# Kernel tuning notes

Measured on AMD Instinct MI355X. Metric: run time of the kernel, lower is better.

The kernel has to match this reference:

```python
import jax, jax.numpy as jnp
import numpy as np

P_CHAN, P_FEAT = 7, 2
S_CHAN, S_FEAT = 2, 4
STATE_SIZE = 8
E, H = 32, 4
ACTIONS = 7
B = 131072


def _lin(x, w, b):
    return x @ w.T + b


def _ln(x, g, b):
    mu = jnp.mean(x, axis=-1, keepdims=True)
    var = jnp.var(x, axis=-1, keepdims=True)
    return (x - mu) * jax.lax.rsqrt(var + 1e-5) * g + b


def _encoder(x, qkv_w, qkv_b, o_w, o_b, g1, b1, f1w, f1b, f2w, f2b, g2, b2):
    # torch.nn.TransformerEncoderLayer, post-norm, relu, dropout=0
    Bn, S, Em = x.shape
    D = Em // H
    qkv = _lin(x, qkv_w, qkv_b)                      # [B,S,3E]
    q, k, v = jnp.split(qkv, 3, axis=-1)
    q = q.reshape(Bn, S, H, D).transpose(0, 2, 1, 3)  # [B,H,S,D]
    k = k.reshape(Bn, S, H, D).transpose(0, 2, 1, 3)
    v = v.reshape(Bn, S, H, D).transpose(0, 2, 1, 3)
    scores = jnp.einsum('bhsd,bhtd->bhst', q, k) * (1.0 / np.sqrt(D))
    att = jax.nn.softmax(scores, axis=-1)
    o = jnp.einsum('bhst,bhtd->bhsd', att, v).transpose(0, 2, 1, 3).reshape(Bn, S, Em)
    x = _ln(x + _lin(o, o_w, o_b), g1, b1)
    ff = _lin(jax.nn.relu(_lin(x, f1w, f1b)), f2w, f2b)
    return _ln(x + ff, g2, b2)


_BRANCH_NAMES = ['in_w', 'in_b', 'qkv_w', 'qkv_b', 'o_w', 'o_b', 'ln1_g', 'ln1_b',
                 'ff1_w', 'ff1_b', 'ff2_w', 'ff2_b', 'ln2_g', 'ln2_b', 'out_w', 'out_b']


def _branch_params(ks, feat, chan):
    def W(shape):
        s = 1.0 / np.sqrt(shape[-1])
        return jax.random.uniform(next(ks), shape, jnp.float32, -s, s)
    return [W((E, feat)), W((E,)), W((3 * E, E)), W((3 * E,)), W((E, E)), W((E,)),
            jnp.ones(E, jnp.float32), jnp.zeros(E, jnp.float32),
            W((E, E)), W((E,)), W((E, E)), W((E,)),
            jnp.ones(E, jnp.float32), jnp.zeros(E, jnp.float32),
            W((128, chan * E)), W((128,))]


def setup_inputs() -> dict:
    key = jax.random.key(0)
    ks = iter(jax.random.split(key, 64))
    def W(shape):
        s = 1.0 / np.sqrt(shape[-1])
        return jax.random.uniform(next(ks), shape, jnp.float32, -s, s)
    d = {'state': jax.random.normal(next(ks), (B, P_CHAN * P_FEAT + S_CHAN * S_FEAT + STATE_SIZE), jnp.float32)}
    d.update({f'pw_{n}': v for n, v in zip(_BRANCH_NAMES, _branch_params(ks, P_FEAT, P_CHAN))})
    d.update({f'sw_{n}': v for n, v in zip(_BRANCH_NAMES, _branch_params(ks, S_FEAT, S_CHAN))})
    d.update(dict(e_w=W((128, STATE_SIZE)), e_b=W((128,)),
                  d1_w=W((128, 384)), d1_b=W((128,)),
                  d2_w=W((128, 128)), d2_b=W((128,)),
                  pi_w=W((ACTIONS, 128)), pi_b=W((ACTIONS,)),
                  v_w=W((1, 128)), v_b=W((1,))))
    return d


def reference(state, pw_in_w, pw_in_b, pw_qkv_w, pw_qkv_b, pw_o_w, pw_o_b, pw_ln1_g, pw_ln1_b,
              pw_ff1_w, pw_ff1_b, pw_ff2_w, pw_ff2_b, pw_ln2_g, pw_ln2_b, pw_out_w, pw_out_b,
              sw_in_w, sw_in_b, sw_qkv_w, sw_qkv_b, sw_o_w, sw_o_b, sw_ln1_g, sw_ln1_b,
              sw_ff1_w, sw_ff1_b, sw_ff2_w, sw_ff2_b, sw_ln2_g, sw_ln2_b, sw_out_w, sw_out_b,
              e_w, e_b, d1_w, d1_b, d2_w, d2_b, pi_w, pi_b, v_w, v_b):
    Bn = state.shape[0]
    power, sword, ps = jnp.split(state, [P_CHAN * P_FEAT, P_CHAN * P_FEAT + S_CHAN * S_FEAT], axis=1)

    p = _lin(power.reshape(Bn * P_CHAN, P_FEAT), pw_in_w, pw_in_b).reshape(Bn, P_CHAN, E)
    p = _encoder(p, pw_qkv_w, pw_qkv_b, pw_o_w, pw_o_b, pw_ln1_g, pw_ln1_b,
                 pw_ff1_w, pw_ff1_b, pw_ff2_w, pw_ff2_b, pw_ln2_g, pw_ln2_b)
    p_emb = jax.nn.relu(_lin(p.reshape(Bn, -1), pw_out_w, pw_out_b))

    s = _lin(sword.reshape(Bn * S_CHAN, S_FEAT), sw_in_w, sw_in_b).reshape(Bn, S_CHAN, E)
    s = _encoder(s, sw_qkv_w, sw_qkv_b, sw_o_w, sw_o_b, sw_ln1_g, sw_ln1_b,
                 sw_ff1_w, sw_ff1_b, sw_ff2_w, sw_ff2_b, sw_ln2_g, sw_ln2_b)
    s_emb = jax.nn.relu(_lin(s.reshape(Bn, -1), sw_out_w, sw_out_b))

    st_emb = jax.nn.relu(_lin(ps, e_w, e_b))
    x = jnp.concatenate([p_emb, s_emb, st_emb], axis=1)  # [B,384]
    x = jax.nn.relu(_lin(x, d1_w, d1_b))
    x = jax.nn.relu(_lin(x, d2_w, d2_b))
    return jax.nn.softmax(_lin(x, pi_w, pi_b), axis=-1), _lin(x, v_w, v_b)
```

## Files before the change

### kernel.cpp

```cpp
#include <hip/hip_runtime.h>


typedef __bf16 bhalf;
typedef __bf16 bhalf4 __attribute__((ext_vector_type(4)));
typedef __bf16 bhalf8 __attribute__((ext_vector_type(8)));
typedef float f32x4 __attribute__((ext_vector_type(4)));
typedef float f32x2 __attribute__((ext_vector_type(2)));

#define DEV static __device__ __forceinline__

DEV f32x4 mfma16(bhalf8 a, bhalf8 b, f32x4 c) {
  return __builtin_amdgcn_mfma_f32_16x16x32_bf16(a, b, c, 0, 0, 0);
}

struct Ptrs {
  const float* state;
  const float *p_g1, *p_b1, *p_f1b, *p_f2b, *p_g2, *p_b2, *p_out_b;
  const float *s_g1, *s_b1, *s_f1b, *s_f2b, *s_g2, *s_b2, *s_out_b;
  const float *d1_b, *d2_b, *pi_w, *pi_b, *v_w, *v_b;
  const bhalf *A_qp, *A_xp, *w_o, *w_f1, *w_f2, *w_out;
  const bhalf *A_qs, *A_xs, *w_o2, *w_f12, *w_f22, *w_out2;
  const bhalf *A_e, *w_d1, *w_d2;
  float* out;
};

struct PrepArgs {
  const float* src[10];
  int len[10];
  int dstOff[10];
  bhalf* dst;
};

__global__ void prep_convert(PrepArgs a) {
  int idx = blockIdx.x * blockDim.x + threadIdx.x;
  int off = 0;
#pragma unroll
  for (int i = 0; i < 10; ++i) {
    int n = a.len[i];
    if (idx >= off && idx < off + n) a.dst[a.dstOff[i] + idx - off] = (bhalf)a.src[i][idx - off];
    off += n;
  }
}

struct EffArgs {
  const float *p_qkv_w, *p_in_w, *p_in_b, *p_qkv_b, *p_o_b;
  const float *s_qkv_w, *s_in_w, *s_in_b, *s_qkv_b, *s_o_b;
  const float *e_w, *e_b;
  bhalf* dst;
};

__global__ void prep_eff(EffArgs a) {
  int tid = threadIdx.x;
  if (tid < 96) {
    const float* wq = a.p_qkv_w + tid * 32;
    float w0 = 0.f, w1 = 0.f, be = 0.f;
    for (int e = 0; e < 32; ++e) {
      w0 += wq[e] * a.p_in_w[e * 2];
      w1 += wq[e] * a.p_in_w[e * 2 + 1];
      be += wq[e] * a.p_in_b[e];
    }
    be += a.p_qkv_b[tid];
    bhalf* d = a.dst + tid * 32;
    for (int k = 0; k < 32; ++k) d[k] = (bhalf)0.f;
    d[0] = (bhalf)w0; d[1] = (bhalf)w1; d[2] = (bhalf)be;
  } else if (tid < 192) {
    int o = tid - 96;
    const float* wq = a.s_qkv_w + o * 32;
    float wf[4] = {0.f, 0.f, 0.f, 0.f}, be = 0.f;
    for (int e = 0; e < 32; ++e) {
      for (int f = 0; f < 4; ++f) wf[f] += wq[e] * a.s_in_w[e * 4 + f];
      be += wq[e] * a.s_in_b[e];
    }
    be += a.s_qkv_b[o];
    bhalf* d = a.dst + 35840 + o * 32;
    for (int k = 0; k < 32; ++k) d[k] = (bhalf)0.f;
    for (int f = 0; f < 4; ++f) d[f] = (bhalf)wf[f];
    d[4] = (bhalf)be;
  } else if (tid < 224) {
    int e = tid - 192;
    bhalf* d = a.dst + 3072 + e * 32;
    for (int k = 0; k < 32; ++k) d[k] = (bhalf)0.f;
    d[0] = (bhalf)a.p_in_w[e * 2];
    d[1] = (bhalf)a.p_in_w[e * 2 + 1];
    d[2] = (bhalf)(a.p_in_b[e] + a.p_o_b[e]);
  } else if (tid < 256) {
    int e = tid - 224;
    bhalf* d = a.dst + 38912 + e * 32;
    for (int k = 0; k < 32; ++k) d[k] = (bhalf)0.f;
    for (int f = 0; f < 4; ++f) d[f] = (bhalf)a.s_in_w[e * 4 + f];
    d[4] = (bhalf)(a.s_in_b[e] + a.s_o_b[e]);
  } else if (tid < 384) {
    int o = tid - 256;
    bhalf* d = a.dst + 51200 + o * 32;
    for (int k = 0; k < 32; ++k) d[k] = (bhalf)0.f;
    for (int k = 0; k < 8; ++k) d[k] = (bhalf)a.e_w[o * 8 + k];
    d[8] = (bhalf)a.e_b[o];
  }
}

template <int T>
DEV bhalf8 attn_head(const bhalf* qkv, int rowbase, int a, int s, int h) {
  const bhalf* base = &qkv[(rowbase + s) * 104 + h * 8];
  const int rstep = 32 * 104;
  bhalf8 kf[T];
#pragma unroll
  for (int b = 0; b < T; ++b) kf[b] = *(const bhalf8*)(base + b * rstep + 32);
  bhalf8 qv = *(const bhalf8*)(base + a * rstep);
  float q[8];
#pragma unroll
  for (int i = 0; i < 8; ++i) q[i] = (float)qv[i];
  float sc[T];
  float mx = -1e30f;
#pragma unroll
  for (int b = 0; b < T; ++b) {
    float d = 0.f;
#pragma unroll
    for (int i = 0; i < 8; ++i) d += q[i] * (float)kf[b][i];
    d *= 0.35355339059327378f;
    sc[b] = d;
    mx = fmaxf(mx, d);
  }
  bhalf8 vf[T];
#pragma unroll
  for (int b = 0; b < T; ++b) vf[b] = *(const bhalf8*)(base + b * rstep + 64);
  float sum = 0.f;
#pragma unroll
  for (int b = 0; b < T; ++b) { sc[b] = __expf(sc[b] - mx); sum += sc[b]; }
  float inv = 1.f / sum;
  float o[8] = {0.f, 0.f, 0.f, 0.f, 0.f, 0.f, 0.f, 0.f};
#pragma unroll
  for (int b = 0; b < T; ++b) {
    float w = sc[b] * inv;
#pragma unroll
    for (int i = 0; i < 8; ++i) o[i] += w * (float)vf[b][i];
  }
  bhalf8 ov;
#pragma unroll
  for (int i = 0; i < 8; ++i) ov[i] = (bhalf)o[i];
  return ov;
}

DEV void ln_pass(int tid, const bhalf* src, bhalf* dst,
                 const float* gp, const float* bp, const float* gs, const float* bs) {
  for (int i = tid; i < 576; i += 512) {
    int row = i >> 1, half = i & 1;
    const bhalf* p = &src[row * 32 + half * 16];
    bhalf8 a0 = *(const bhalf8*)p;
    bhalf8 a1 = *(const bhalf8*)(p + 8);
    float v[16];
#pragma unroll
    for (int k = 0; k < 8; ++k) { v[k] = (float)a0[k]; v[8 + k] = (float)a1[k]; }
    float sum = 0.f, ss = 0.f;
#pragma unroll
    for (int k = 0; k < 16; ++k) { sum += v[k]; ss += v[k] * v[k]; }
    sum += __shfl_xor(sum, 1);
    ss += __shfl_xor(ss, 1);
    float mu = sum * 0.03125f;
    float rs = rsqrtf(ss * 0.03125f - mu * mu + 1e-5f);
    const float* g = (row < 224 ? gp : gs) + half * 16;
    const float* b = (row < 224 ? bp : bs) + half * 16;
    bhalf8 o0, o1;
#pragma unroll
    for (int k = 0; k < 8; ++k) {
      o0[k] = (bhalf)((v[k] - mu) * rs * g[k] + b[k]);
      o1[k] = (bhalf)((v[8 + k] - mu) * rs * g[8 + k] + b[8 + k]);
    }
    bhalf* q = &dst[row * 32 + half * 16];
    *(bhalf8*)q = o0;
    *(bhalf8*)(q + 8) = o1;
  }
}

__launch_bounds__(512, 4)
__global__ void aac_main(Ptrs P) {
  __shared__ __align__(16) bhalf s_x[288 * 32];
  __shared__ __align__(16) bhalf s_q[288 * 104];

  bhalf* ff1 = s_q;
  bhalf* xcat = s_q;
  bhalf* h1 = s_q + 13056;
  float* h2 = (float*)(s_q + 17408);

  const int tid = threadIdx.x;
  const int wave = tid >> 6, lane = tid & 63;
  const int l15 = lane & 15, lq = lane >> 4;
  const int s0 = blockIdx.x * 32;

  for (int f = wave; f < 144; f += 8) {
    int tile, n;
    bool isQ = f < 108;
    if (isQ) { tile = f / 6; n = f - tile * 6; }
    else { int g = f - 108; tile = g >> 1; n = g & 1; }
    bhalf8 bf;
#pragma unroll
    for (int k = 0; k < 8; ++k) bf[k] = (bhalf)0.f;
    if (lq == 0) {
      if (tile < 14) {
        int t = tile >> 1, s = (tile & 1) * 16 + l15;
        f32x2 v = *(const f32x2*)&P.state[(size_t)(s0 + s) * 30 + 2 * t];
        bf[0] = (bhalf)v[0]; bf[1] = (bhalf)v[1]; bf[2] = (bhalf)1.0f;
      } else {
        int g2 = tile - 14, ts = g2 >> 1, s = (g2 & 1) * 16 + l15;
        const float* st = &P.state[(size_t)(s0 + s) * 30 + 14 + 4 * ts];
        f32x2 v0 = *(const f32x2*)st;
        f32x2 v1 = *(const f32x2*)(st + 2);
        bf[0] = (bhalf)v0[0]; bf[1] = (bhalf)v0[1];
        bf[2] = (bhalf)v1[0]; bf[3] = (bhalf)v1[1];
        bf[4] = (bhalf)1.0f;
      }
    }
    const bhalf* aptr;
    if (isQ) aptr = (tile < 14 ? P.A_qp : P.A_qs) + (n * 16 + l15) * 32 + lq * 8;
    else     aptr = (tile < 14 ? P.A_xp : P.A_xs) + (n * 16 + l15) * 32 + lq * 8;
    f32x4 c = {0.f, 0.f, 0.f, 0.f};
    c = mfma16(*(const bhalf8*)aptr, bf, c);
    bhalf4 o;
#pragma unroll
    for (int j = 0; j < 4; ++j) o[j] = (bhalf)c[j];
    int row = tile * 16 + l15;
    if (isQ) *(bhalf4*)&s_q[row * 104 + n * 16 + lq * 4] = o;
    else     *(bhalf4*)&s_x[row * 32 + n * 16 + lq * 4] = o;
  }
  __syncthreads();

  for (int tile = wave; tile < 18; tile += 8) {
    bhalf8 ov;
    const bhalf* wo;
    if (tile < 14) {
      ov = attn_head<7>(s_q, 0, tile >> 1, (tile & 1) * 16 + l15, lq);
      wo = P.w_o;
    } else {
      int g = tile - 14;
      ov = attn_head<2>(s_q, 224, g >> 1, (g & 1) * 16 + l15, lq);
      wo = P.w_o2;
    }
    int row = tile * 16 + l15;
    bhalf4 x0 = *(const bhalf4*)&s_x[row * 32 + lq * 4];
    bhalf4 x1 = *(const bhalf4*)&s_x[row * 32 + 16 + lq * 4];
    f32x4 c0, c1;
#pragma unroll
    for (int j = 0; j < 4; ++j) { c0[j] = (float)x0[j]; c1[j] = (float)x1[j]; }
    c0 = mfma16(*(const bhalf8*)&wo[l15 * 32 + lq * 8], ov, c0);
    c1 = mfma16(*(const bhalf8*)&wo[(16 + l15) * 32 + lq * 8], ov, c1);
    bhalf4 p0, p1;
#pragma unroll
    for (int j = 0; j < 4; ++j) { p0[j] = (bhalf)c0[j]; p1[j] = (bhalf)c1[j]; }
    *(bhalf4*)&s_x[row * 32 + lq * 4] = p0;
    *(bhalf4*)&s_x[row * 32 + 16 + lq * 4] = p1;
  }
  __syncthreads();

  ln_pass(tid, s_x, s_x, P.p_g1, P.p_b1, P.s_g1, P.s_b1);
  __syncthreads();

  for (int tile = wave; tile < 18; tile += 8) {
    const bhalf* wf = tile < 14 ? P.w_f1 : P.w_f12;
    const float* fb = tile < 14 ? P.p_f1b : P.s_f1b;
    int row = tile * 16 + l15;
    bhalf8 bfr = *(const bhalf8*)&s_x[row * 32 + lq * 8];
    f32x4 c0 = {0.f, 0.f, 0.f, 0.f}, c1 = {0.f, 0.f, 0.f, 0.f};
    c0 = mfma16(*(const bhalf8*)&wf[l15 * 32 + lq * 8], bfr, c0);
    c1 = mfma16(*(const bhalf8*)&wf[(16 + l15) * 32 + lq * 8], bfr, c1);
    f32x4 b0 = *(const f32x4*)&fb[lq * 4], b1 = *(const f32x4*)&fb[16 + lq * 4];
    bhalf4 p0, p1;
#pragma unroll
    for (int j = 0; j < 4; ++j) {
      p0[j] = (bhalf)fmaxf(c0[j] + b0[j], 0.f);
      p1[j] = (bhalf)fmaxf(c1[j] + b1[j], 0.f);
    }
    *(bhalf4*)&ff1[row * 32 + lq * 4] = p0;
    *(bhalf4*)&ff1[row * 32 + 16 + lq * 4] = p1;
  }
  __syncthreads();

  for (int tile = wave; tile < 18; tile += 8) {
    const bhalf* wf = tile < 14 ? P.w_f2 : P.w_f22;
    const float* fb = tile < 14 ? P.p_f2b : P.s_f2b;
    int row = tile * 16 + l15;
    bhalf8 bfr = *(const bhalf8*)&ff1[row * 32 + lq * 8];
    bhalf4 r0 = *(const bhalf4*)&s_x[row * 32 + lq * 4];
    bhalf4 r1 = *(const bhalf4*)&s_x[row * 32 + 16 + lq * 4];
    f32x4 b0 = *(const f32x4*)&fb[lq * 4], b1 = *(const f32x4*)&fb[16 + lq * 4];
    f32x4 c0, c1;
#pragma unroll
    for (int j = 0; j < 4; ++j) {
      c0[j] = b0[j] + (float)r0[j];
      c1[j] = b1[j] + (float)r1[j];
    }
    c0 = mfma16(*(const bhalf8*)&wf[l15 * 32 + lq * 8], bfr, c0);
    c1 = mfma16(*(const bhalf8*)&wf[(16 + l15) * 32 + lq * 8], bfr, c1);
    bhalf4 p0, p1;
#pragma unroll
    for (int j = 0; j < 4; ++j) { p0[j] = (bhalf)c0[j]; p1[j] = (bhalf)c1[j]; }
    *(bhalf4*)&ff1[row * 32 + lq * 4] = p0;
    *(bhalf4*)&ff1[row * 32 + 16 + lq * 4] = p1;
  }
  __syncthreads();

  ln_pass(tid, ff1, s_x, P.p_g2, P.p_b2, P.s_g2, P.s_b2);
  __syncthreads();

  for (int f = wave; f < 48; f += 8) {
    if (f < 16) {
      int n = f >> 1, m = f & 1;
      f32x4 c = {0.f, 0.f, 0.f, 0.f};
#pragma unroll
      for (int t = 0; t < 7; ++t) {
        bhalf8 a = *(const bhalf8*)&P.w_out[(n * 16 + l15) * 224 + t * 32 + lq * 8];
        bhalf8 b = *(const bhalf8*)&s_x[(t * 32 + m * 16 + l15) * 32 + lq * 8];
        c = mfma16(a, b, c);
      }
      int oc = n * 16 + lq * 4;
      f32x4 bias = *(const f32x4*)&P.p_out_b[oc];
      bhalf4 o;
#pragma unroll
      for (int j = 0; j < 4; ++j) o[j] = (bhalf)fmaxf(c[j] + bias[j], 0.f);
      *(bhalf4*)&xcat[(m * 16 + l15) * 408 + oc] = o;
    } else if (f < 32) {
      int g = f - 16, n = g >> 1, m = g & 1;
      f32x4 c = {0.f, 0.f, 0.f, 0.f};
#pragma unroll
      for (int t = 0; t < 2; ++t) {
        bhalf8 a = *(const bhalf8*)&P.w_out2[(n * 16 + l15) * 64 + t * 32 + lq * 8];
        bhalf8 b = *(const bhalf8*)&s_x[(224 + t * 32 + m * 16 + l15) * 32 + lq * 8];
        c = mfma16(a, b, c);
      }
      int oc = n * 16 + lq * 4;
      f32x4 bias = *(const f32x4*)&P.s_out_b[oc];
      bhalf4 o;
#pragma unroll
      for (int j = 0; j < 4; ++j) o[j] = (bhalf)fmaxf(c[j] + bias[j], 0.f);
      *(bhalf4*)&xcat[(m * 16 + l15) * 408 + 128 + oc] = o;
    } else {
      int g = f - 32, n = g >> 1, m = g & 1;
      int s = m * 16 + l15;
      bhalf8 bf;
#pragma unroll
      for (int k = 0; k < 8; ++k) bf[k] = (bhalf)0.f;
      if (lq == 0) {
        const float* st = &P.state[(size_t)(s0 + s) * 30 + 22];
#pragma unroll
        for (int k = 0; k < 4; ++k) {
          f32x2 v = *(const f32x2*)(st + 2 * k);
          bf[2 * k] = (bhalf)v[0];
          bf[2 * k + 1] = (bhalf)v[1];
        }
      } else if (lq == 1) {
        bf[0] = (bhalf)1.0f;
      }
      bhalf8 a = *(const bhalf8*)&P.A_e[(n * 16 + l15) * 32 + lq * 8];
      f32x4 c = {0.f, 0.f, 0.f, 0.f};
      c = mfma16(a, bf, c);
      bhalf4 o;
#pragma unroll
      for (int j = 0; j < 4; ++j) o[j] = (bhalf)fmaxf(c[j], 0.f);
      *(bhalf4*)&xcat[s * 408 + 256 + n * 16 + lq * 4] = o;
    }
  }
  __syncthreads();

  for (int f = wave; f < 16; f += 8) {
    int m = f >> 3, n = f & 7;
    f32x4 c = {0.f, 0.f, 0.f, 0.f};
#pragma unroll
    for (int ks = 0; ks < 12; ++ks) {
      bhalf8 a = *(const bhalf8*)&P.w_d1[(n * 16 + l15) * 384 + ks * 32 + lq * 8];
      bhalf8 b = *(const bhalf8*)&xcat[(m * 16 + l15) * 408 + ks * 32 + lq * 8];
      c = mfma16(a, b, c);
    }
    int oc = n * 16 + lq * 4;
    f32x4 bias = *(const f32x4*)&P.d1_b[oc];
    bhalf4 o;
#pragma unroll
    for (int j = 0; j < 4; ++j) o[j] = (bhalf)fmaxf(c[j] + bias[j], 0.f);
    *(bhalf4*)&h1[(m * 16 + l15) * 136 + oc] = o;
  }
  __syncthreads();

  for (int f = wave; f < 16; f += 8) {
    int m = f >> 3, n = f & 7;
    f32x4 c = {0.f, 0.f, 0.f, 0.f};
#pragma unroll
    for (int ks = 0; ks < 4; ++ks) {
      bhalf8 a = *(const bhalf8*)&P.w_d2[(n * 16 + l15) * 128 + ks * 32 + lq * 8];
      bhalf8 b = *(const bhalf8*)&h1[(m * 16 + l15) * 136 + ks * 32 + lq * 8];
      c = mfma16(a, b, c);
    }
    int oc = n * 16 + lq * 4;
    f32x4 bias = *(const f32x4*)&P.d2_b[oc];
    f32x4 o;
#pragma unroll
    for (int j = 0; j < 4; ++j) o[j] = fmaxf(c[j] + bias[j], 0.f);
    *(f32x4*)&h2[(m * 16 + l15) * 140 + oc] = o;
  }
  __syncthreads();

  if (tid < 256) {
    int s = tid >> 3, o = tid & 7;
    const float* wrow = (o < 7) ? &P.pi_w[o * 128] : P.v_w;
    const float* hrow = &h2[s * 140];
    float acc = (o < 7) ? P.pi_b[o] : P.v_b[0];
#pragma unroll
    for (int k = 0; k < 32; ++k) {
      f32x4 wv = *(const f32x4*)&wrow[k * 4];
      f32x4 hv = *(const f32x4*)&hrow[k * 4];
#pragma unroll
      for (int j = 0; j < 4; ++j) acc += wv[j] * hv[j];
    }
    float xm = (o < 7) ? acc : -1e30f;
#pragma unroll
    for (int m = 1; m < 8; m <<= 1) xm = fmaxf(xm, __shfl_xor(xm, m));
    float e = (o < 7) ? __expf(acc - xm) : 0.f;
    float se = e;
#pragma unroll
    for (int m = 1; m < 8; m <<= 1) se += __shfl_xor(se, m);
    if (o < 7) P.out[(size_t)(s0 + s) * 7 + o] = e / se;
    else       P.out[917504 + s0 + s] = acc;
  }
}

extern "C" void kernel_launch(void* const* d_in, const int* in_sizes, int n_in,
                              void* d_out, int out_size, void* d_ws, size_t ws_size,
                              hipStream_t stream) {
  (void)in_sizes; (void)n_in; (void)out_size; (void)ws_size;
  const float* const* in = (const float* const*)d_in;
  bhalf* wbf = (bhalf*)d_ws;

  PrepArgs pa;
  const int srcIdx[10] = {5, 9, 11, 15, 21, 25, 27, 31, 35, 37};
  const int lens[10] = {1024, 1024, 1024, 28672, 1024, 1024, 1024, 8192, 49152, 16384};
  const int dsts[10] = {4096, 5120, 6144, 7168, 39936, 40960, 41984, 43008, 55296, 104448};
  for (int i = 0; i < 10; ++i) { pa.src[i] = in[srcIdx[i]]; pa.len[i] = lens[i]; pa.dstOff[i] = dsts[i]; }
  pa.dst = wbf;
  hipLaunchKernelGGL(prep_convert, dim3(424), dim3(256), 0, stream, pa);

  EffArgs ea;
  ea.p_qkv_w = in[3]; ea.p_in_w = in[1]; ea.p_in_b = in[2]; ea.p_qkv_b = in[4]; ea.p_o_b = in[6];
  ea.s_qkv_w = in[19]; ea.s_in_w = in[17]; ea.s_in_b = in[18]; ea.s_qkv_b = in[20]; ea.s_o_b = in[22];
  ea.e_w = in[33]; ea.e_b = in[34];
  ea.dst = wbf;
  hipLaunchKernelGGL(prep_eff, dim3(1), dim3(384), 0, stream, ea);

  Ptrs P;
  P.state = in[0];
  P.p_g1 = in[7];  P.p_b1 = in[8];  P.p_f1b = in[10]; P.p_f2b = in[12];
  P.p_g2 = in[13]; P.p_b2 = in[14]; P.p_out_b = in[16];
  P.s_g1 = in[23]; P.s_b1 = in[24]; P.s_f1b = in[26]; P.s_f2b = in[28];
  P.s_g2 = in[29]; P.s_b2 = in[30]; P.s_out_b = in[32];
  P.d1_b = in[36]; P.d2_b = in[38];
  P.pi_w = in[39]; P.pi_b = in[40]; P.v_w = in[41]; P.v_b = in[42];
  P.A_qp = wbf;          P.A_xp = wbf + 3072;   P.w_o = wbf + 4096;
  P.w_f1 = wbf + 5120;   P.w_f2 = wbf + 6144;   P.w_out = wbf + 7168;
  P.A_qs = wbf + 35840;  P.A_xs = wbf + 38912;  P.w_o2 = wbf + 39936;
  P.w_f12 = wbf + 40960; P.w_f22 = wbf + 41984; P.w_out2 = wbf + 43008;
  P.A_e = wbf + 51200;   P.w_d1 = wbf + 55296;  P.w_d2 = wbf + 104448;
  P.out = (float*)d_out;

  hipLaunchKernelGGL(aac_main, dim3(4096), dim3(512), 0, stream, P);
}
```

Measured before the change: 334.6 us.

## Fuse per-tile encoder stages into one wave-local pass with swizzled LDS

Merges attention output projection, LayerNorm 1, FF1, FF2 and LayerNorm 2 into a single per-tile routine that each wave runs on its own 16-row tile. LayerNorm is computed from the MFMA accumulators with cross-lane shuffles instead of a separate block-wide pass. This removes four block-wide __syncthreads and the intermediate LDS round trips. It also XOR-swizzles the s_x layout to reduce bank conflicts and statically unrolls the later output-projection and dense loops per wave. In exchange, work is unevenly spread across waves (waves 0-1 take three tiles, the rest two) and register pressure in the fused routine goes up.

```diff
diff --git a/kernel.cpp b/kernel.cpp
--- a/kernel.cpp
+++ b/kernel.cpp
@@ -12,6 +12,8 @@
 DEV f32x4 mfma16(bhalf8 a, bhalf8 b, f32x4 c) {
   return __builtin_amdgcn_mfma_f32_16x16x32_bf16(a, b, c, 0, 0, 0);
 }
+
+DEV int sxo(int row, int col) { return row * 32 + (col ^ ((row & 3) << 3)); }
 
 struct Ptrs {
   const float* state;
@@ -140,35 +142,77 @@
   return ov;
 }
 
-DEV void ln_pass(int tid, const bhalf* src, bhalf* dst,
-                 const float* gp, const float* bp, const float* gs, const float* bs) {
-  for (int i = tid; i < 576; i += 512) {
-    int row = i >> 1, half = i & 1;
-    const bhalf* p = &src[row * 32 + half * 16];
-    bhalf8 a0 = *(const bhalf8*)p;
-    bhalf8 a1 = *(const bhalf8*)(p + 8);
-    float v[16];
-#pragma unroll
-    for (int k = 0; k < 8; ++k) { v[k] = (float)a0[k]; v[8 + k] = (float)a1[k]; }
-    float sum = 0.f, ss = 0.f;
-#pragma unroll
-    for (int k = 0; k < 16; ++k) { sum += v[k]; ss += v[k] * v[k]; }
-    sum += __shfl_xor(sum, 1);
-    ss += __shfl_xor(ss, 1);
-    float mu = sum * 0.03125f;
-    float rs = rsqrtf(ss * 0.03125f - mu * mu + 1e-5f);
-    const float* g = (row < 224 ? gp : gs) + half * 16;
-    const float* b = (row < 224 ? bp : bs) + half * 16;
-    bhalf8 o0, o1;
-#pragma unroll
-    for (int k = 0; k < 8; ++k) {
-      o0[k] = (bhalf)((v[k] - mu) * rs * g[k] + b[k]);
-      o1[k] = (bhalf)((v[8 + k] - mu) * rs * g[8 + k] + b[8 + k]);
-    }
-    bhalf* q = &dst[row * 32 + half * 16];
-    *(bhalf8*)q = o0;
-    *(bhalf8*)(q + 8) = o1;
-  }
+template <int T>
+DEV void enc_tile(const bhalf* s_q, bhalf* s_x, int tile, int rowbase, int a,
+                  int l15, int lq,
+                  const bhalf* wo, const bhalf* wf1, const bhalf* wf2,
+                  const float* g1, const float* b1, const float* f1b,
+                  const float* f2b, const float* g2, const float* b2) {
+  const int s = (tile & 1) * 16 + l15;
+  bhalf8 ov = attn_head<T>(s_q, rowbase, a, s, lq);
+  const int row = tile * 16 + l15;
+  bhalf4 x0 = *(const bhalf4*)&s_x[sxo(row, lq * 4)];
+  bhalf4 x1 = *(const bhalf4*)&s_x[sxo(row, 16 + lq * 4)];
+  f32x4 c0, c1;
+#pragma unroll
+  for (int j = 0; j < 4; ++j) { c0[j] = (float)x0[j]; c1[j] = (float)x1[j]; }
+  c0 = mfma16(*(const bhalf8*)&wo[l15 * 32 + lq * 8], ov, c0);
+  c1 = mfma16(*(const bhalf8*)&wo[(16 + l15) * 32 + lq * 8], ov, c1);
+  float sum = 0.f, ss = 0.f;
+#pragma unroll
+  for (int j = 0; j < 4; ++j) { sum += c0[j] + c1[j]; ss += c0[j] * c0[j] + c1[j] * c1[j]; }
+  sum += __shfl_xor(sum, 16); sum += __shfl_xor(sum, 32);
+  ss += __shfl_xor(ss, 16); ss += __shfl_xor(ss, 32);
+  float mu = sum * 0.03125f;
+  float rs = rsqrtf(ss * 0.03125f - mu * mu + 1e-5f);
+  f32x4 gg0 = *(const f32x4*)&g1[lq * 4], gg1 = *(const f32x4*)&g1[16 + lq * 4];
+  f32x4 hb0 = *(const f32x4*)&b1[lq * 4], hb1 = *(const f32x4*)&b1[16 + lq * 4];
+  float xn[8];
+#pragma unroll
+  for (int j = 0; j < 4; ++j) {
+    xn[j] = (c0[j] - mu) * rs * gg0[j] + hb0[j];
+    xn[4 + j] = (c1[j] - mu) * rs * gg1[j] + hb1[j];
+  }
+  bhalf4 p0, p1;
+#pragma unroll
+  for (int j = 0; j < 4; ++j) { p0[j] = (bhalf)xn[j]; p1[j] = (bhalf)xn[4 + j]; }
+  *(bhalf4*)&s_x[sxo(row, lq * 4)] = p0;
+  *(bhalf4*)&s_x[sxo(row, 16 + lq * 4)] = p1;
+  bhalf8 bfr = *(const bhalf8*)&s_x[sxo(row, lq * 8)];
+  c0 = f32x4{0.f, 0.f, 0.f, 0.f};
+  c1 = f32x4{0.f, 0.f, 0.f, 0.f};
+  c0 = mfma16(*(const bhalf8*)&wf1[l15 * 32 + lq * 8], bfr, c0);
+  c1 = mfma16(*(const bhalf8*)&wf1[(16 + l15) * 32 + lq * 8], bfr, c1);
+  f32x4 fb0 = *(const f32x4*)&f1b[lq * 4], fb1 = *(const f32x4*)&f1b[16 + lq * 4];
+#pragma unroll
+  for (int j = 0; j < 4; ++j) {
+    p0[j] = (bhalf)fmaxf(c0[j] + fb0[j], 0.f);
+    p1[j] = (bhalf)fmaxf(c1[j] + fb1[j], 0.f);
+  }
+  *(bhalf4*)&s_x[sxo(row, lq * 4)] = p0;
+  *(bhalf4*)&s_x[sxo(row, 16 + lq * 4)] = p1;
+  bfr = *(const bhalf8*)&s_x[sxo(row, lq * 8)];
+  f32x4 f20 = *(const f32x4*)&f2b[lq * 4], f21 = *(const f32x4*)&f2b[16 + lq * 4];
+#pragma unroll
+  for (int j = 0; j < 4; ++j) { c0[j] = xn[j] + f20[j]; c1[j] = xn[4 + j] + f21[j]; }
+  c0 = mfma16(*(const bhalf8*)&wf2[l15 * 32 + lq * 8], bfr, c0);
+  c1 = mfma16(*(const bhalf8*)&wf2[(16 + l15) * 32 + lq * 8], bfr, c1);
+  sum = 0.f; ss = 0.f;
+#pragma unroll
+  for (int j = 0; j < 4; ++j) { sum += c0[j] + c1[j]; ss += c0[j] * c0[j] + c1[j] * c1[j]; }
+  sum += __shfl_xor(sum, 16); sum += __shfl_xor(sum, 32);
+  ss += __shfl_xor(ss, 16); ss += __shfl_xor(ss, 32);
+  mu = sum * 0.03125f;
+  rs = rsqrtf(ss * 0.03125f - mu * mu + 1e-5f);
+  f32x4 g20 = *(const f32x4*)&g2[lq * 4], g21 = *(const f32x4*)&g2[16 + lq * 4];
+  f32x4 b20 = *(const f32x4*)&b2[lq * 4], b21 = *(const f32x4*)&b2[16 + lq * 4];
+#pragma unroll
+  for (int j = 0; j < 4; ++j) {
+    p0[j] = (bhalf)((c0[j] - mu) * rs * g20[j] + b20[j]);
+    p1[j] = (bhalf)((c1[j] - mu) * rs * g21[j] + b21[j]);
+  }
+  *(bhalf4*)&s_x[sxo(row, lq * 4)] = p0;
+  *(bhalf4*)&s_x[sxo(row, 16 + lq * 4)] = p1;
 }
 
 __launch_bounds__(512, 4)
@@ -176,7 +220,6 @@
   __shared__ __align__(16) bhalf s_x[288 * 32];
   __shared__ __align__(16) bhalf s_q[288 * 104];
 
-  bhalf* ff1 = s_q;
   bhalf* xcat = s_q;
   bhalf* h1 = s_q + 13056;
   float* h2 = (float*)(s_q + 17408);
@@ -219,148 +262,95 @@
     for (int j = 0; j < 4; ++j) o[j] = (bhalf)c[j];
     int row = tile * 16 + l15;
     if (isQ) *(bhalf4*)&s_q[row * 104 + n * 16 + lq * 4] = o;
-    else     *(bhalf4*)&s_x[row * 32 + n * 16 + lq * 4] = o;
+    else     *(bhalf4*)&s_x[sxo(row, n * 16 + lq * 4)] = o;
   }
   __syncthreads();
 
-  for (int tile = wave; tile < 18; tile += 8) {
-    bhalf8 ov;
-    const bhalf* wo;
-    if (tile < 14) {
-      ov = attn_head<7>(s_q, 0, tile >> 1, (tile & 1) * 16 + l15, lq);
-      wo = P.w_o;
+  {
+    enc_tile<7>(s_q, s_x, wave, 0, wave >> 1, l15, lq,
+                P.w_o, P.w_f1, P.w_f2, P.p_g1, P.p_b1, P.p_f1b, P.p_f2b, P.p_g2, P.p_b2);
+    if (wave < 6) {
+      enc_tile<7>(s_q, s_x, wave + 8, 0, (wave + 8) >> 1, l15, lq,
+                  P.w_o, P.w_f1, P.w_f2, P.p_g1, P.p_b1, P.p_f1b, P.p_f2b, P.p_g2, P.p_b2);
     } else {
-      int g = tile - 14;
-      ov = attn_head<2>(s_q, 224, g >> 1, (g & 1) * 16 + l15, lq);
-      wo = P.w_o2;
-    }
-    int row = tile * 16 + l15;
-    bhalf4 x0 = *(const bhalf4*)&s_x[row * 32 + lq * 4];
-    bhalf4 x1 = *(const bhalf4*)&s_x[row * 32 + 16 + lq * 4];
-    f32x4 c0, c1;
-#pragma unroll
-    for (int j = 0; j < 4; ++j) { c0[j] = (float)x0[j]; c1[j] = (float)x1[j]; }
-    c0 = mfma16(*(const bhalf8*)&wo[l15 * 32 + lq * 8], ov, c0);
-    c1 = mfma16(*(const bhalf8*)&wo[(16 + l15) * 32 + lq * 8], ov, c1);
-    bhalf4 p0, p1;
-#pragma unroll
-    for (int j = 0; j < 4; ++j) { p0[j] = (bhalf)c0[j]; p1[j] = (bhalf)c1[j]; }
-    *(bhalf4*)&s_x[row * 32 + lq * 4] = p0;
-    *(bhalf4*)&s_x[row * 32 + 16 + lq * 4] = p1;
+      enc_tile<2>(s_q, s_x, wave + 8, 224, (wave + 8 - 14) >> 1, l15, lq,
+                  P.w_o2, P.w_f12, P.w_f22, P.s_g1, P.s_b1, P.s_f1b, P.s_f2b, P.s_g2, P.s_b2);
+    }
+    if (wave < 2) {
+      enc_tile<2>(s_q, s_x, 16 + wave, 224, (16 + wave - 14) >> 1, l15, lq,
+                  P.w_o2, P.w_f12, P.w_f22, P.s_g1, P.s_b1, P.s_f1b, P.s_f2b, P.s_g2, P.s_b2);
+    }
   }
   __syncthreads();
 
-  ln_pass(tid, s_x, s_x, P.p_g1, P.p_b1, P.s_g1, P.s_b1);
+#pragma unroll
+  for (int k = 0; k < 2; ++k) {
+    int f = wave + 8 * k;
+    int n = f >> 1, m = f & 1;
+    f32x4 c = {0.f, 0.f, 0.f, 0.f};
+#pragma unroll
+    for (int t = 0; t < 7; ++t) {
+      bhalf8 a = *(const bhalf8*)&P.w_out[(n * 16 + l15) * 224 + t * 32 + lq * 8];
+      bhalf8 b = *(const bhalf8*)&s_x[sxo(t * 32 + m * 16 + l15, lq * 8)];
+      c = mfma16(a, b, c);
+    }
+    int oc = n * 16 + lq * 4;
+    f32x4 bias = *(const f32x4*)&P.p_out_b[oc];
+    bhalf4 o;
+#pragma unroll
+    for (int j = 0; j < 4; ++j) o[j] = (bhalf)fmaxf(c[j] + bias[j], 0.f);
+    *(bhalf4*)&xcat[(m * 16 + l15) * 408 + oc] = o;
+  }
+#pragma unroll
+  for (int k = 0; k < 2; ++k) {
+    int g = wave + 8 * k;
+    int n = g >> 1, m = g & 1;
+    f32x4 c = {0.f, 0.f, 0.f, 0.f};
+#pragma unroll
+    for (int t = 0; t < 2; ++t) {
+      bhalf8 a = *(const bhalf8*)&P.w_out2[(n * 16 + l15) * 64 + t * 32 + lq * 8];
+      bhalf8 b = *(const bhalf8*)&s_x[sxo(224 + t * 32 + m * 16 + l15, lq * 8)];
+      c = mfma16(a, b, c);
+    }
+    int oc = n * 16 + lq * 4;
+    f32x4 bias = *(const f32x4*)&P.s_out_b[oc];
+    bhalf4 o;
+#pragma unroll
+    for (int j = 0; j < 4; ++j) o[j] = (bhalf)fmaxf(c[j] + bias[j], 0.f);
+    *(bhalf4*)&xcat[(m * 16 + l15) * 408 + 128 + oc] = o;
+  }
+#pragma unroll
+  for (int k = 0; k < 2; ++k) {
+    int g = wave + 8 * k;
+    int n = g >> 1, m = g & 1;
+    int s = m * 16 + l15;
+    bhalf8 bf;
+#pragma unroll
+    for (int kk = 0; kk < 8; ++kk) bf[kk] = (bhalf)0.f;
+    if (lq == 0) {
+      const float* st = &P.state[(size_t)(s0 + s) * 30 + 22];
+#pragma unroll
+      for (int kk = 0; kk < 4; ++kk) {
+        f32x2 v = *(const f32x2*)(st + 2 * kk);
+        bf[2 * kk] = (bhalf)v[0];
+        bf[2 * kk + 1] = (bhalf)v[1];
+      }
+    } else if (lq == 1) {
+      bf[0] = (bhalf)1.0f;
+    }
+    bhalf8 a = *(const bhalf8*)&P.A_e[(n * 16 + l15) * 32 + lq * 8];
+    f32x4 c = {0.f, 0.f, 0.f, 0.f};
+    c = mfma16(a, bf, c);
+    bhalf4 o;
+#pragma unroll
+    for (int j = 0; j < 4; ++j) o[j] = (bhalf)fmaxf(c[j], 0.f);
+    *(bhalf4*)&xcat[s * 408 + 256 + n * 16 + lq * 4] = o;
+  }
   __syncthreads();
 
-  for (int tile = wave; tile < 18; tile += 8) {
-    const bhalf* wf = tile < 14 ? P.w_f1 : P.w_f12;
-    const float* fb = tile < 14 ? P.p_f1b : P.s_f1b;
-    int row = tile * 16 + l15;
-    bhalf8 bfr = *(const bhalf8*)&s_x[row * 32 + lq * 8];
-    f32x4 c0 = {0.f, 0.f, 0.f, 0.f}, c1 = {0.f, 0.f, 0.f, 0.f};
-    c0 = mfma16(*(const bhalf8*)&wf[l15 * 32 + lq * 8], bfr, c0);
-    c1 = mfma16(*(const bhalf8*)&wf[(16 + l15) * 32 + lq * 8], bfr, c1);
-    f32x4 b0 = *(const f32x4*)&fb[lq * 4], b1 = *(const f32x4*)&fb[16 + lq * 4];
-    bhalf4 p0, p1;
-#pragma unroll
-    for (int j = 0; j < 4; ++j) {
-      p0[j] = (bhalf)fmaxf(c0[j] + b0[j], 0.f);
-      p1[j] = (bhalf)fmaxf(c1[j] + b1[j], 0.f);
-    }
-    *(bhalf4*)&ff1[row * 32 + lq * 4] = p0;
-    *(bhalf4*)&ff1[row * 32 + 16 + lq * 4] = p1;
-  }
-  __syncthreads();
-
-  for (int tile = wave; tile < 18; tile += 8) {
-    const bhalf* wf = tile < 14 ? P.w_f2 : P.w_f22;
-    const float* fb = tile < 14 ? P.p_f2b : P.s_f2b;
-    int row = tile * 16 + l15;
-    bhalf8 bfr = *(const bhalf8*)&ff1[row * 32 + lq * 8];
-    bhalf4 r0 = *(const bhalf4*)&s_x[row * 32 + lq * 4];
-    bhalf4 r1 = *(const bhalf4*)&s_x[row * 32 + 16 + lq * 4];
-    f32x4 b0 = *(const f32x4*)&fb[lq * 4], b1 = *(const f32x4*)&fb[16 + lq * 4];
-    f32x4 c0, c1;
-#pragma unroll
-    for (int j = 0; j < 4; ++j) {
-      c0[j] = b0[j] + (float)r0[j];
-      c1[j] = b1[j] + (float)r1[j];
-    }
-    c0 = mfma16(*(const bhalf8*)&wf[l15 * 32 + lq * 8], bfr, c0);
-    c1 = mfma16(*(const bhalf8*)&wf[(16 + l15) * 32 + lq * 8], bfr, c1);
-    bhalf4 p0, p1;
-#pragma unroll
-    for (int j = 0; j < 4; ++j) { p0[j] = (bhalf)c0[j]; p1[j] = (bhalf)c1[j]; }
-    *(bhalf4*)&ff1[row * 32 + lq * 4] = p0;
-    *(bhalf4*)&ff1[row * 32 + 16 + lq * 4] = p1;
-  }
-  __syncthreads();
-
-  ln_pass(tid, ff1, s_x, P.p_g2, P.p_b2, P.s_g2, P.s_b2);
-  __syncthreads();
-
-  for (int f = wave; f < 48; f += 8) {
-    if (f < 16) {
-      int n = f >> 1, m = f & 1;
-      f32x4 c = {0.f, 0.f, 0.f, 0.f};
-#pragma unroll
-      for (int t = 0; t < 7; ++t) {
-        bhalf8 a = *(const bhalf8*)&P.w_out[(n * 16 + l15) * 224 + t * 32 + lq * 8];
-        bhalf8 b = *(const bhalf8*)&s_x[(t * 32 + m * 16 + l15) * 32 + lq * 8];
-        c = mfma16(a, b, c);
-      }
-      int oc = n * 16 + lq * 4;
-      f32x4 bias = *(const f32x4*)&P.p_out_b[oc];
-      bhalf4 o;
-#pragma unroll
-      for (int j = 0; j < 4; ++j) o[j] = (bhalf)fmaxf(c[j] + bias[j], 0.f);
-      *(bhalf4*)&xcat[(m * 16 + l15) * 408 + oc] = o;
-    } else if (f < 32) {
-      int g = f - 16, n = g >> 1, m = g & 1;
-      f32x4 c = {0.f, 0.f, 0.f, 0.f};
-#pragma unroll
-      for (int t = 0; t < 2; ++t) {
-        bhalf8 a = *(const bhalf8*)&P.w_out2[(n * 16 + l15) * 64 + t * 32 + lq * 8];
-        bhalf8 b = *(const bhalf8*)&s_x[(224 + t * 32 + m * 16 + l15) * 32 + lq * 8];
-        c = mfma16(a, b, c);
-      }
-      int oc = n * 16 + lq * 4;
-      f32x4 bias = *(const f32x4*)&P.s_out_b[oc];
-      bhalf4 o;
-#pragma unroll
-      for (int j = 0; j < 4; ++j) o[j] = (bhalf)fmaxf(c[j] + bias[j], 0.f);
-      *(bhalf4*)&xcat[(m * 16 + l15) * 408 + 128 + oc] = o;
-    } else {
-      int g = f - 32, n = g >> 1, m = g & 1;
-      int s = m * 16 + l15;
-      bhalf8 bf;
-#pragma unroll
-      for (int k = 0; k < 8; ++k) bf[k] = (bhalf)0.f;
-      if (lq == 0) {
-        const float* st = &P.state[(size_t)(s0 + s) * 30 + 22];
-#pragma unroll
-        for (int k = 0; k < 4; ++k) {
-          f32x2 v = *(const f32x2*)(st + 2 * k);
-          bf[2 * k] = (bhalf)v[0];
-          bf[2 * k + 1] = (bhalf)v[1];
-        }
-      } else if (lq == 1) {
-        bf[0] = (bhalf)1.0f;
-      }
-      bhalf8 a = *(const bhalf8*)&P.A_e[(n * 16 + l15) * 32 + lq * 8];
-      f32x4 c = {0.f, 0.f, 0.f, 0.f};
-      c = mfma16(a, bf, c);
-      bhalf4 o;
-#pragma unroll
-      for (int j = 0; j < 4; ++j) o[j] = (bhalf)fmaxf(c[j], 0.f);
-      *(bhalf4*)&xcat[s * 408 + 256 + n * 16 + lq * 4] = o;
-    }
-  }
-  __syncthreads();
-
-  for (int f = wave; f < 16; f += 8) {
-    int m = f >> 3, n = f & 7;
+#pragma unroll
+  for (int m = 0; m < 2; ++m) {
+    int n = wave;
     f32x4 c = {0.f, 0.f, 0.f, 0.f};
 #pragma unroll
     for (int ks = 0; ks < 12; ++ks) {
@@ -377,8 +367,9 @@
   }
   __syncthreads();
 
-  for (int f = wave; f < 16; f += 8) {
-    int m = f >> 3, n = f & 7;
+#pragma unroll
+  for (int m = 0; m < 2; ++m) {
+    int n = wave;
     f32x4 c = {0.f, 0.f, 0.f, 0.f};
 #pragma unroll
     for (int ks = 0; ks < 4; ++ks) {
```

Result: faster. 319.1 us (-4.6%).
